# Performance work log

Hardware: AMD Instinct MI355X
Metric: run time of the kernel (lower is better)

Reference implementation:

```python
import jax, jax.numpy as jnp
import numpy as np

N = 100000
E = 1600000
EPS = 1e-16
NEG_SLOPE = 0.2


def setup_inputs() -> dict:
    key = jax.random.key(0)
    ks = jax.random.split(key, 10)
    F_in, C = 512, 40
    H1, D1 = 8, 8
    return {
        "x": jax.random.normal(ks[0], (N, F_in), jnp.float32),
        "edge_index": jax.random.randint(ks[1], (2, E), 0, N, jnp.int64),
        "W1": jax.random.normal(ks[2], (F_in, H1 * D1), jnp.float32) * 0.05,
        "att_src1": jax.random.normal(ks[3], (H1, D1), jnp.float32) * 0.1,
        "att_dst1": jax.random.normal(ks[4], (H1, D1), jnp.float32) * 0.1,
        "b1": jnp.zeros((H1 * D1,), jnp.float32),
        "W2": jax.random.normal(ks[5], (H1 * D1, C), jnp.float32) * 0.05,
        "att_src2": jax.random.normal(ks[6], (1, C), jnp.float32) * 0.1,
        "att_dst2": jax.random.normal(ks[7], (1, C), jnp.float32) * 0.1,
        "b2": jnp.zeros((C,), jnp.float32),
    }


def gat_conv(x, W, att_src, att_dst, bias, src, dst, heads, out_dim, concat):
    # Linear transform per head: [N, H, D]
    h = (x @ W).reshape(N, heads, out_dim)
    # Per-node attention logits: [N, H]
    a_src = jnp.einsum("nhd,hd->nh", h, att_src)
    a_dst = jnp.einsum("nhd,hd->nh", h, att_dst)
    # Per-edge logits (edge j->i: src=j, softmax grouped by dst=i)
    e = a_src[src] + a_dst[dst]                      # [E', H]
    e = jax.nn.leaky_relu(e, NEG_SLOPE)
    # Segment softmax over destination nodes (numerically stable)
    m = jax.ops.segment_max(e, dst, num_segments=N)  # [N, H]
    e = jnp.exp(e - m[dst])
    s = jax.ops.segment_sum(e, dst, num_segments=N)  # [N, H]
    alpha = e / (s[dst] + EPS)                       # [E', H]
    # Weighted message aggregation (scatter-add)
    msg = h[src] * alpha[:, :, None]                 # [E', H, D]
    out = jax.ops.segment_sum(msg, dst, num_segments=N)  # [N, H, D]
    out = out.reshape(N, heads * out_dim) if concat else out.mean(axis=1)
    return out + bias


def reference(x, edge_index, W1, att_src1, att_dst1, b1, W2, att_src2, att_dst2, b2):
    # PyG GATConv default: add self-loops
    loops = jnp.arange(N, dtype=edge_index.dtype)
    src = jnp.concatenate([edge_index[0], loops])
    dst = jnp.concatenate([edge_index[1], loops])
    h = gat_conv(x, W1, att_src1, att_dst1, b1, src, dst, heads=8, out_dim=8, concat=True)
    h = jax.nn.elu(h)
    out = gat_conv(h, W2, att_src2, att_dst2, b2, src, dst, heads=1, out_dim=40, concat=False)
    return jax.nn.log_softmax(out, axis=1)
```

## Files before the change

### kernel.cpp

```cpp
#include <hip/hip_runtime.h>
#include <cstdint>

#define N_NODES 100000
#define N_EDGES 1600000
#define ETOT    1700000
#define FIN     512
#define HD1     64
#define C2      40
#define NEG_SLOPE 0.2f
#define SCAN_NB ((N_NODES + 1023) / 1024)

typedef __attribute__((ext_vector_type(8))) short bf16x8;
typedef __attribute__((ext_vector_type(4))) float f32x4;

__device__ __forceinline__ float lrelu(float v) { return v > 0.f ? v : NEG_SLOPE * v; }

__device__ __forceinline__ unsigned short f2bf(float f) {
    uint32_t u = __float_as_uint(f);
    u += 0x7FFF + ((u >> 16) & 1);
    return (unsigned short)(u >> 16);
}
__device__ __forceinline__ float bf2f(unsigned short u) {
    return __uint_as_float(((uint32_t)u) << 16);
}

__global__ void k_prep(const float* __restrict__ W1, const float* __restrict__ a_s,
                       const float* __restrict__ a_d,
                       const float* __restrict__ W2, const float* __restrict__ att_s2,
                       const float* __restrict__ att_d2,
                       unsigned short* __restrict__ W1t, unsigned short* __restrict__ W2t,
                       int* __restrict__ deg) {
    int i = blockIdx.x * 256 + threadIdx.x;
    if (i < N_NODES) deg[i] = 0;
    if (i < 80 * 512) {
        int n = i >> 9, k = i & 511;
        float v;
        if (n < 64) {
            v = W1[k * HD1 + n];
        } else if (n < 72) {
            int h = n - 64; v = 0.f;
#pragma unroll
            for (int d = 0; d < 8; d++) v += W1[k * HD1 + h * 8 + d] * a_s[h * 8 + d];
        } else {
            int h = n - 72; v = 0.f;
#pragma unroll
            for (int d = 0; d < 8; d++) v += W1[k * HD1 + h * 8 + d] * a_d[h * 8 + d];
        }
        W1t[n * FIN + k] = f2bf(v);
    } else if (i < 80 * 512 + 48 * 64) {
        int j = i - 80 * 512;
        int n = j >> 6, k = j & 63;
        float v = 0.f;
        if (n < C2) {
            v = W2[k * C2 + n];
        } else if (n == C2) {
            for (int c = 0; c < C2; c++) v += W2[k * C2 + c] * att_s2[c];
        } else if (n == C2 + 1) {
            for (int c = 0; c < C2; c++) v += W2[k * C2 + c] * att_d2[c];
        }
        W2t[n * 64 + k] = f2bf(v);
    }
}

__global__ __launch_bounds__(256) void k_gemm1(const float* __restrict__ x,
                                               const unsigned short* __restrict__ W1t,
                                               unsigned short* __restrict__ h1b,
                                               float* __restrict__ as1,
                                               float* __restrict__ ad1) {
    __shared__ unsigned short As[128 * 72];
    const int t    = threadIdx.x;
    const int lane = t & 63, wv = t >> 6;
    const int quad = lane >> 4, l16 = lane & 15;
    const int row0 = blockIdx.x * 128;

    f32x4 acc[2][5];
#pragma unroll
    for (int mi = 0; mi < 2; mi++)
#pragma unroll
        for (int ni = 0; ni < 5; ni++) acc[mi][ni] = (f32x4){0.f, 0.f, 0.f, 0.f};

    float4 rx[8];
#pragma unroll
    for (int i = 0; i < 8; i++) {
        int ff = t + i * 256;
        int r = ff >> 4, c4 = ff & 15;
        int row = row0 + r;
        rx[i] = (row < N_NODES) ? *(const float4*)&x[(size_t)row * FIN + c4 * 4]
                                : make_float4(0.f, 0.f, 0.f, 0.f);
    }

    for (int c = 0; c < 8; c++) {
#pragma unroll
        for (int i = 0; i < 8; i++) {
            int ff = t + i * 256;
            int r = ff >> 4, c4 = ff & 15;
            ushort4 s4;
            s4.x = f2bf(rx[i].x); s4.y = f2bf(rx[i].y);
            s4.z = f2bf(rx[i].z); s4.w = f2bf(rx[i].w);
            *(ushort4*)&As[r * 72 + c4 * 4] = s4;
        }
        __syncthreads();
        if (c < 7) {
            int kb = (c + 1) * 64;
#pragma unroll
            for (int i = 0; i < 8; i++) {
                int ff = t + i * 256;
                int r = ff >> 4, c4 = ff & 15;
                int row = row0 + r;
                rx[i] = (row < N_NODES) ? *(const float4*)&x[(size_t)row * FIN + kb + c4 * 4]
                                        : make_float4(0.f, 0.f, 0.f, 0.f);
            }
        }
        int kb = c * 64;
#pragma unroll
        for (int ks = 0; ks < 2; ks++) {
            bf16x8 af[2], bfv[5];
#pragma unroll
            for (int mi = 0; mi < 2; mi++) {
                int lr = wv * 32 + mi * 16 + l16;
                af[mi] = *(const bf16x8*)&As[lr * 72 + ks * 32 + quad * 8];
            }
#pragma unroll
            for (int ni = 0; ni < 5; ni++) {
                int n = ni * 16 + l16;
                bfv[ni] = *(const bf16x8*)&W1t[n * FIN + kb + ks * 32 + quad * 8];
            }
#pragma unroll
            for (int mi = 0; mi < 2; mi++)
#pragma unroll
                for (int ni = 0; ni < 5; ni++)
                    acc[mi][ni] = __builtin_amdgcn_mfma_f32_16x16x32_bf16(
                        af[mi], bfv[ni], acc[mi][ni], 0, 0, 0);
        }
        __syncthreads();
    }
#pragma unroll
    for (int mi = 0; mi < 2; mi++)
#pragma unroll
        for (int ni = 0; ni < 5; ni++)
#pragma unroll
            for (int r = 0; r < 4; r++) {
                int row = row0 + wv * 32 + mi * 16 + quad * 4 + r;
                if (row >= N_NODES) continue;
                int col = ni * 16 + l16;
                float v = acc[mi][ni][r];
                if (col < 64)       h1b[(size_t)row * 64 + col] = f2bf(v);
                else if (col < 72)  as1[row * 8 + (col - 64)] = v;
                else                ad1[row * 8 + (col - 72)] = v;
            }
}

__global__ void k_degord(const int* __restrict__ ei, int* __restrict__ deg,
                         int* __restrict__ ord) {
    int e = blockIdx.x * 256 + threadIdx.x;
    if (e >= ETOT) return;
    int dst = (e < N_EDGES) ? ei[N_EDGES + e] : e - N_EDGES;
    ord[e] = atomicAdd(&deg[dst], 1);
}

__global__ __launch_bounds__(1024) void k_bsum(const int* __restrict__ deg,
                                               int* __restrict__ bsum) {
    __shared__ int wsm[16];
    int t = threadIdx.x;
    int i = blockIdx.x * 1024 + t;
    int v = (i < N_NODES) ? deg[i] : 0;
#pragma unroll
    for (int o = 32; o >= 1; o >>= 1) v += __shfl_xor(v, o, 64);
    if ((t & 63) == 0) wsm[t >> 6] = v;
    __syncthreads();
    if (t < 16) {
        int s = wsm[t];
#pragma unroll
        for (int o = 8; o >= 1; o >>= 1) s += __shfl_xor(s, o, 16);
        if (t == 0) bsum[blockIdx.x] = s;
    }
}

__global__ __launch_bounds__(128) void k_bscan(const int* __restrict__ bsum,
                                               int* __restrict__ boff) {
    __shared__ int sh[128];
    int t = threadIdx.x;
    int v = (t < SCAN_NB) ? bsum[t] : 0;
    sh[t] = v;
    __syncthreads();
    for (int off = 1; off < 128; off <<= 1) {
        int u = (t >= off) ? sh[t - off] : 0;
        __syncthreads();
        sh[t] += u;
        __syncthreads();
    }
    boff[t] = sh[t] - v;
}

__global__ __launch_bounds__(1024) void k_scan3(const int* __restrict__ deg,
                                                const int* __restrict__ boff,
                                                int* __restrict__ row_ptr) {
    __shared__ int sh[1024];
    int t = threadIdx.x;
    int i = blockIdx.x * 1024 + t;
    int v = (i < N_NODES) ? deg[i] : 0;
    sh[t] = v;
    __syncthreads();
    for (int off = 1; off < 1024; off <<= 1) {
        int u = (t >= off) ? sh[t - off] : 0;
        __syncthreads();
        sh[t] += u;
        __syncthreads();
    }
    int base = boff[blockIdx.x];
    if (i < N_NODES) row_ptr[i] = base + sh[t] - v;
    if (i == N_NODES - 1) row_ptr[N_NODES] = base + sh[t];
}

__global__ void k_scatter(const int* __restrict__ ei, const int* __restrict__ row_ptr,
                          const int* __restrict__ ord, int* __restrict__ csr_src) {
    int e = blockIdx.x * 256 + threadIdx.x;
    if (e >= ETOT) return;
    int src, dst;
    if (e < N_EDGES) { src = ei[e]; dst = ei[N_EDGES + e]; }
    else             { src = dst = e - N_EDGES; }
    csr_src[row_ptr[dst] + ord[e]] = src;
}

__global__ __launch_bounds__(256) void k_agg1(
    const unsigned short* __restrict__ h1b,
    const float* __restrict__ as1, const float* __restrict__ ad1,
    const int* __restrict__ row_ptr, const int* __restrict__ csr_src,
    const float* __restrict__ b1, unsigned short* __restrict__ hb) {
    int t = threadIdx.x, wv = t >> 6, lane = t & 63;
    int dst = blockIdx.x * 4 + wv;
    if (dst >= N_NODES) return;
    int g = lane >> 3, i8 = lane & 7;
    int s0 = row_ptr[dst], s1e = row_ptr[dst + 1];
    float adh = ad1[dst * 8 + i8];
    float den = 0.f;
    float facc[8];
#pragma unroll
    for (int d = 0; d < 8; d++) facc[d] = 0.f;

    for (int base = s0; base < s1e; base += 64) {
        int idx = base + lane;
        int sl = (idx < s1e) ? csr_src[idx] : 0;
        int cnt = min(64, s1e - base);
        for (int j = 0; j < cnt; j += 8) {
            int s = __shfl(sl, j + g);
            bool vld = (j + g) < cnt;
            float w = vld ? __expf(lrelu(as1[s * 8 + i8] + adh)) : 0.f;
            den += w;
            bf16x8 hrow = *(const bf16x8*)&h1b[(size_t)s * 64 + i8 * 8];
#pragma unroll
            for (int d = 0; d < 8; d++)
                facc[d] += w * bf2f((unsigned short)hrow[d]);
        }
    }
#pragma unroll
    for (int o = 8; o <= 32; o <<= 1) {
        den += __shfl_xor(den, o, 64);
#pragma unroll
        for (int d = 0; d < 8; d++) facc[d] += __shfl_xor(facc[d], o, 64);
    }
    float rden = 1.f / (den + 1e-16f);
    float4 b1lo = *(const float4*)&b1[i8 * 8];
    float4 b1hi = *(const float4*)&b1[i8 * 8 + 4];
    float bb[8] = {b1lo.x, b1lo.y, b1lo.z, b1lo.w, b1hi.x, b1hi.y, b1hi.z, b1hi.w};
    bf16x8 pk;
#pragma unroll
    for (int d = 0; d < 8; d++) {
        float hv = facc[d] * rden + bb[d];
        hv = hv > 0.f ? hv : expm1f(hv);
        pk[d] = (short)f2bf(hv);
    }
    if (g == 0) *(bf16x8*)&hb[(size_t)dst * 64 + i8 * 8] = pk;
}

__global__ __launch_bounds__(256) void k_gemm2(const unsigned short* __restrict__ hb,
                                               const unsigned short* __restrict__ W2t,
                                               unsigned short* __restrict__ h2b,
                                               float* __restrict__ as2,
                                               float* __restrict__ ad2) {
    const int t = threadIdx.x;
    const int lane = t & 63, wv = t >> 6;
    const int quad = lane >> 4, l16 = lane & 15;
    const int row0 = blockIdx.x * 128;

    f32x4 acc[2][3];
#pragma unroll
    for (int mi = 0; mi < 2; mi++)
#pragma unroll
        for (int ni = 0; ni < 3; ni++) acc[mi][ni] = (f32x4){0.f, 0.f, 0.f, 0.f};

    bf16x8 bfrag[2][3];
#pragma unroll
    for (int ks = 0; ks < 2; ks++)
#pragma unroll
        for (int ni = 0; ni < 3; ni++)
            bfrag[ks][ni] = *(const bf16x8*)&W2t[(ni * 16 + l16) * 64 + ks * 32 + quad * 8];

#pragma unroll
    for (int mi = 0; mi < 2; mi++) {
        int row = row0 + wv * 32 + mi * 16 + l16;
        int rowc = row < N_NODES ? row : N_NODES - 1;
#pragma unroll
        for (int ks = 0; ks < 2; ks++) {
            bf16x8 af = *(const bf16x8*)&hb[(size_t)rowc * 64 + ks * 32 + quad * 8];
#pragma unroll
            for (int ni = 0; ni < 3; ni++)
                acc[mi][ni] = __builtin_amdgcn_mfma_f32_16x16x32_bf16(
                    af, bfrag[ks][ni], acc[mi][ni], 0, 0, 0);
        }
    }
#pragma unroll
    for (int mi = 0; mi < 2; mi++)
#pragma unroll
        for (int ni = 0; ni < 3; ni++)
#pragma unroll
            for (int r = 0; r < 4; r++) {
                int row = row0 + wv * 32 + mi * 16 + quad * 4 + r;
                if (row >= N_NODES) continue;
                int col = ni * 16 + l16;
                float v = acc[mi][ni][r];
                if (col < C2)            h2b[(size_t)row * C2 + col] = f2bf(v);
                else if (col == C2)      as2[row] = v;
                else if (col == C2 + 1)  ad2[row] = v;
            }
}

__global__ __launch_bounds__(256) void k_agg2(
    const unsigned short* __restrict__ h2b,
    const float* __restrict__ as2, const float* __restrict__ ad2,
    const int* __restrict__ row_ptr, const int* __restrict__ csr_src,
    const float* __restrict__ b2, float* __restrict__ out) {
    int t = threadIdx.x, wv = t >> 6, lane = t & 63;
    int dst = blockIdx.x * 4 + wv;
    if (dst >= N_NODES) return;
    int g = lane >> 3, i8 = lane & 7;
    bool act = i8 < 5;
    int off = act ? i8 * 8 : 0;
    int s0 = row_ptr[dst], s1e = row_ptr[dst + 1];
    float ad = ad2[dst];
    float denp = 0.f;
    float facc[8];
#pragma unroll
    for (int d = 0; d < 8; d++) facc[d] = 0.f;

    for (int base = s0; base < s1e; base += 64) {
        int idx = base + lane;
        int sl = (idx < s1e) ? csr_src[idx] : 0;
        int cnt = min(64, s1e - base);
        for (int j = 0; j < cnt; j += 8) {
            int s = __shfl(sl, j + g);
            bool vld = (j + g) < cnt;
            float wf = vld ? __expf(lrelu(as2[s] + ad)) : 0.f;
            if (i8 == 0) denp += wf;
            float w = act ? wf : 0.f;
            bf16x8 hrow = *(const bf16x8*)&h2b[(size_t)s * C2 + off];
#pragma unroll
            for (int d = 0; d < 8; d++)
                facc[d] += w * bf2f((unsigned short)hrow[d]);
        }
    }
#pragma unroll
    for (int o = 8; o <= 32; o <<= 1)
#pragma unroll
        for (int d = 0; d < 8; d++) facc[d] += __shfl_xor(facc[d], o, 64);
    float den = denp;
#pragma unroll
    for (int o = 32; o >= 1; o >>= 1) den += __shfl_xor(den, o, 64);
    float rden = 1.f / (den + 1e-16f);

    float vch[8];
    float mx = -1e30f;
#pragma unroll
    for (int d = 0; d < 8; d++) {
        vch[d] = act ? facc[d] * rden + b2[off + d] : -1e30f;
        mx = fmaxf(mx, vch[d]);
    }
#pragma unroll
    for (int o = 1; o <= 4; o <<= 1) mx = fmaxf(mx, __shfl_xor(mx, o, 64));
    float es = 0.f;
#pragma unroll
    for (int d = 0; d < 8; d++) es += act ? __expf(vch[d] - mx) : 0.f;
#pragma unroll
    for (int o = 1; o <= 4; o <<= 1) es += __shfl_xor(es, o, 64);
    float lg = logf(es);
    if (g == 0 && act) {
        float4 o0 = {vch[0] - mx - lg, vch[1] - mx - lg, vch[2] - mx - lg, vch[3] - mx - lg};
        float4 o1 = {vch[4] - mx - lg, vch[5] - mx - lg, vch[6] - mx - lg, vch[7] - mx - lg};
        *(float4*)&out[(size_t)dst * C2 + i8 * 8]     = o0;
        *(float4*)&out[(size_t)dst * C2 + i8 * 8 + 4] = o1;
    }
}

extern "C" void kernel_launch(void* const* d_in, const int* in_sizes, int n_in,
                              void* d_out, int out_size, void* d_ws, size_t ws_size,
                              hipStream_t stream) {
    const float* x     = (const float*)d_in[0];
    const int*   ei    = (const int*)d_in[1];
    const float* W1    = (const float*)d_in[2];
    const float* at_s1 = (const float*)d_in[3];
    const float* at_d1 = (const float*)d_in[4];
    const float* b1    = (const float*)d_in[5];
    const float* W2    = (const float*)d_in[6];
    const float* at_s2 = (const float*)d_in[7];
    const float* at_d2 = (const float*)d_in[8];
    const float* b2    = (const float*)d_in[9];
    float* out = (float*)d_out;
    float* ws  = (float*)d_ws;

    unsigned short* h1b = (unsigned short*)ws;
    float* as1 = ws + 3200000;
    float* ad1 = ws + 4000000;
    unsigned short* hb  = (unsigned short*)(ws + 4800000);
    unsigned short* h2b = (unsigned short*)(ws + 8000000);
    float* as2 = ws + 10000000;
    float* ad2 = ws + 10100000;
    unsigned short* W1t = (unsigned short*)(ws + 10200000);
    unsigned short* W2t = (unsigned short*)(ws + 10250000);
    int* row_ptr = (int*)(ws + 10300000);
    int* deg     = (int*)(ws + 10410000);
    int* csr_src = (int*)(ws + 10630000);
    int* bsum    = (int*)(ws + 12340000);
    int* boff    = (int*)(ws + 12350000);
    int* ord     = (int*)(ws + 13000000);

    k_prep<<<391, 256, 0, stream>>>(W1, at_s1, at_d1, W2, at_s2, at_d2, W1t, W2t, deg);
    k_degord<<<(ETOT + 255) / 256, 256, 0, stream>>>(ei, deg, ord);
    k_bsum<<<SCAN_NB, 1024, 0, stream>>>(deg, bsum);
    k_bscan<<<1, 128, 0, stream>>>(bsum, boff);
    k_scan3<<<SCAN_NB, 1024, 0, stream>>>(deg, boff, row_ptr);
    k_scatter<<<(ETOT + 255) / 256, 256, 0, stream>>>(ei, row_ptr, ord, csr_src);
    k_gemm1<<<(N_NODES + 127) / 128, 256, 0, stream>>>(x, W1t, h1b, as1, ad1);
    k_agg1<<<(N_NODES + 3) / 4, 256, 0, stream>>>(h1b, as1, ad1, row_ptr, csr_src, b1, hb);
    k_gemm2<<<(N_NODES + 127) / 128, 256, 0, stream>>>(hb, W2t, h2b, as2, ad2);
    k_agg2<<<(N_NODES + 3) / 4, 256, 0, stream>>>(h2b, as2, ad2, row_ptr, csr_src, b2, out);
}
```

Before: 593.6 us.

## Fuse degree counting into GEMM1 launch, single-pass lookback scan, unroll aggregation

Merges the edge-degree atomic counting into the GEMM1 kernel as extra blocks, so the bandwidth-bound GEMM and the atomic-bound counting run concurrently in one launch. Replaces the three-kernel scan (block sums, block-sum scan, final scan) with a single decoupled-lookback scan that spins on per-block flags. The aggregation loops in both layers now process two neighbours per iteration to expose more memory-level parallelism. The lookback relies on earlier blocks being scheduled first, which holds for 98 blocks on this device. The two-neighbour loop also raises register pressure.

```diff
diff --git a/kernel.cpp b/kernel.cpp
--- a/kernel.cpp
+++ b/kernel.cpp
@@ -8,7 +8,9 @@
 #define HD1     64
 #define C2      40
 #define NEG_SLOPE 0.2f
-#define SCAN_NB ((N_NODES + 1023) / 1024)
+#define GEMM1_NB 782
+#define DEG_NB   832
+#define SCAN_NB2 98
 
 typedef __attribute__((ext_vector_type(8))) short bf16x8;
 typedef __attribute__((ext_vector_type(4))) float f32x4;
@@ -29,9 +31,10 @@
                        const float* __restrict__ W2, const float* __restrict__ att_s2,
                        const float* __restrict__ att_d2,
                        unsigned short* __restrict__ W1t, unsigned short* __restrict__ W2t,
-                       int* __restrict__ deg) {
+                       int* __restrict__ deg, unsigned int* __restrict__ flags) {
     int i = blockIdx.x * 256 + threadIdx.x;
     if (i < N_NODES) deg[i] = 0;
+    if (i < 128) flags[i] = 0u;
     if (i < 80 * 512) {
         int n = i >> 9, k = i & 511;
         float v;
@@ -62,13 +65,23 @@
     }
 }
 
-__global__ __launch_bounds__(256) void k_gemm1(const float* __restrict__ x,
+__global__ __launch_bounds__(256) void k_g1deg(const float* __restrict__ x,
                                                const unsigned short* __restrict__ W1t,
                                                unsigned short* __restrict__ h1b,
                                                float* __restrict__ as1,
-                                               float* __restrict__ ad1) {
+                                               float* __restrict__ ad1,
+                                               const int* __restrict__ ei,
+                                               int* __restrict__ deg,
+                                               int* __restrict__ ord) {
     __shared__ unsigned short As[128 * 72];
-    const int t    = threadIdx.x;
+    const int t = threadIdx.x;
+    if (blockIdx.x >= GEMM1_NB) {
+        for (int e = ((int)blockIdx.x - GEMM1_NB) * 256 + t; e < ETOT; e += DEG_NB * 256) {
+            int dst = (e < N_EDGES) ? ei[N_EDGES + e] : e - N_EDGES;
+            ord[e] = atomicAdd(&deg[dst], 1);
+        }
+        return;
+    }
     const int lane = t & 63, wv = t >> 6;
     const int quad = lane >> 4, l16 = lane & 15;
     const int row0 = blockIdx.x * 128;
@@ -150,54 +163,15 @@
             }
 }
 
-__global__ void k_degord(const int* __restrict__ ei, int* __restrict__ deg,
-                         int* __restrict__ ord) {
-    int e = blockIdx.x * 256 + threadIdx.x;
-    if (e >= ETOT) return;
-    int dst = (e < N_EDGES) ? ei[N_EDGES + e] : e - N_EDGES;
-    ord[e] = atomicAdd(&deg[dst], 1);
-}
-
-__global__ __launch_bounds__(1024) void k_bsum(const int* __restrict__ deg,
-                                               int* __restrict__ bsum) {
-    __shared__ int wsm[16];
-    int t = threadIdx.x;
-    int i = blockIdx.x * 1024 + t;
-    int v = (i < N_NODES) ? deg[i] : 0;
-#pragma unroll
-    for (int o = 32; o >= 1; o >>= 1) v += __shfl_xor(v, o, 64);
-    if ((t & 63) == 0) wsm[t >> 6] = v;
-    __syncthreads();
-    if (t < 16) {
-        int s = wsm[t];
-#pragma unroll
-        for (int o = 8; o >= 1; o >>= 1) s += __shfl_xor(s, o, 16);
-        if (t == 0) bsum[blockIdx.x] = s;
-    }
-}
-
-__global__ __launch_bounds__(128) void k_bscan(const int* __restrict__ bsum,
-                                               int* __restrict__ boff) {
-    __shared__ int sh[128];
-    int t = threadIdx.x;
-    int v = (t < SCAN_NB) ? bsum[t] : 0;
-    sh[t] = v;
-    __syncthreads();
-    for (int off = 1; off < 128; off <<= 1) {
-        int u = (t >= off) ? sh[t - off] : 0;
-        __syncthreads();
-        sh[t] += u;
-        __syncthreads();
-    }
-    boff[t] = sh[t] - v;
-}
-
-__global__ __launch_bounds__(1024) void k_scan3(const int* __restrict__ deg,
-                                                const int* __restrict__ boff,
-                                                int* __restrict__ row_ptr) {
+__global__ __launch_bounds__(1024) void k_scan_lb(const int* __restrict__ deg,
+                                                  int* __restrict__ row_ptr,
+                                                  int* __restrict__ aggr,
+                                                  int* __restrict__ incl,
+                                                  unsigned int* __restrict__ flags) {
     __shared__ int sh[1024];
-    int t = threadIdx.x;
-    int i = blockIdx.x * 1024 + t;
+    __shared__ int shbase;
+    const int t = threadIdx.x, b = blockIdx.x;
+    const int i = b * 1024 + t;
     int v = (i < N_NODES) ? deg[i] : 0;
     sh[t] = v;
     __syncthreads();
@@ -207,9 +181,39 @@
         sh[t] += u;
         __syncthreads();
     }
-    int base = boff[blockIdx.x];
+    if (t == 0) {
+        int total = sh[1023];
+        int run = 0;
+        if (b == 0) {
+            __hip_atomic_store(&incl[0], total, __ATOMIC_RELEASE, __HIP_MEMORY_SCOPE_AGENT);
+            __hip_atomic_store(&flags[0], 2u, __ATOMIC_RELEASE, __HIP_MEMORY_SCOPE_AGENT);
+        } else {
+            __hip_atomic_store(&aggr[b], total, __ATOMIC_RELEASE, __HIP_MEMORY_SCOPE_AGENT);
+            __hip_atomic_store(&flags[b], 1u, __ATOMIC_RELEASE, __HIP_MEMORY_SCOPE_AGENT);
+            int p = b - 1;
+            while (true) {
+                unsigned int f = __hip_atomic_load(&flags[p], __ATOMIC_ACQUIRE,
+                                                   __HIP_MEMORY_SCOPE_AGENT);
+                if (f == 2u) {
+                    run += __hip_atomic_load(&incl[p], __ATOMIC_ACQUIRE,
+                                             __HIP_MEMORY_SCOPE_AGENT);
+                    break;
+                } else if (f == 1u) {
+                    run += __hip_atomic_load(&aggr[p], __ATOMIC_ACQUIRE,
+                                             __HIP_MEMORY_SCOPE_AGENT);
+                    --p;
+                }
+            }
+            __hip_atomic_store(&incl[b], run + total, __ATOMIC_RELEASE,
+                               __HIP_MEMORY_SCOPE_AGENT);
+            __hip_atomic_store(&flags[b], 2u, __ATOMIC_RELEASE, __HIP_MEMORY_SCOPE_AGENT);
+        }
+        shbase = run;
+        if (b == 0) row_ptr[N_NODES] = ETOT;
+    }
+    __syncthreads();
+    int base = shbase;
     if (i < N_NODES) row_ptr[i] = base + sh[t] - v;
-    if (i == N_NODES - 1) row_ptr[N_NODES] = base + sh[t];
 }
 
 __global__ void k_scatter(const int* __restrict__ ei, const int* __restrict__ row_ptr,
@@ -242,15 +246,21 @@
         int idx = base + lane;
         int sl = (idx < s1e) ? csr_src[idx] : 0;
         int cnt = min(64, s1e - base);
-        for (int j = 0; j < cnt; j += 8) {
-            int s = __shfl(sl, j + g);
-            bool vld = (j + g) < cnt;
-            float w = vld ? __expf(lrelu(as1[s * 8 + i8] + adh)) : 0.f;
-            den += w;
-            bf16x8 hrow = *(const bf16x8*)&h1b[(size_t)s * 64 + i8 * 8];
+        for (int j = 0; j < cnt; j += 16) {
+            int sA = __shfl(sl, j + g);
+            int sB = __shfl(sl, j + 8 + g);
+            bool vA = (j + g) < cnt, vB = (j + 8 + g) < cnt;
+            bf16x8 rA = *(const bf16x8*)&h1b[(size_t)sA * 64 + i8 * 8];
+            bf16x8 rB = *(const bf16x8*)&h1b[(size_t)sB * 64 + i8 * 8];
+            float aA = as1[sA * 8 + i8];
+            float aB = as1[sB * 8 + i8];
+            float wA = vA ? __expf(lrelu(aA + adh)) : 0.f;
+            float wB = vB ? __expf(lrelu(aB + adh)) : 0.f;
+            den += wA + wB;
 #pragma unroll
             for (int d = 0; d < 8; d++)
-                facc[d] += w * bf2f((unsigned short)hrow[d]);
+                facc[d] += wA * bf2f((unsigned short)rA[d]) +
+                           wB * bf2f((unsigned short)rB[d]);
         }
     }
 #pragma unroll
@@ -347,16 +357,23 @@
         int idx = base + lane;
         int sl = (idx < s1e) ? csr_src[idx] : 0;
         int cnt = min(64, s1e - base);
-        for (int j = 0; j < cnt; j += 8) {
-            int s = __shfl(sl, j + g);
-            bool vld = (j + g) < cnt;
-            float wf = vld ? __expf(lrelu(as2[s] + ad)) : 0.f;
-            if (i8 == 0) denp += wf;
-            float w = act ? wf : 0.f;
-            bf16x8 hrow = *(const bf16x8*)&h2b[(size_t)s * C2 + off];
+        for (int j = 0; j < cnt; j += 16) {
+            int sA = __shfl(sl, j + g);
+            int sB = __shfl(sl, j + 8 + g);
+            bool vA = (j + g) < cnt, vB = (j + 8 + g) < cnt;
+            bf16x8 rA = *(const bf16x8*)&h2b[(size_t)sA * C2 + off];
+            bf16x8 rB = *(const bf16x8*)&h2b[(size_t)sB * C2 + off];
+            float aA = as2[sA];
+            float aB = as2[sB];
+            float wfA = vA ? __expf(lrelu(aA + ad)) : 0.f;
+            float wfB = vB ? __expf(lrelu(aB + ad)) : 0.f;
+            if (i8 == 0) denp += wfA + wfB;
+            float wA = act ? wfA : 0.f;
+            float wB = act ? wfB : 0.f;
 #pragma unroll
             for (int d = 0; d < 8; d++)
-                facc[d] += w * bf2f((unsigned short)hrow[d]);
+                facc[d] += wA * bf2f((unsigned short)rA[d]) +
+                           wB * bf2f((unsigned short)rB[d]);
         }
     }
 #pragma unroll
@@ -419,17 +436,15 @@
     int* row_ptr = (int*)(ws + 10300000);
     int* deg     = (int*)(ws + 10410000);
     int* csr_src = (int*)(ws + 10630000);
-    int* bsum    = (int*)(ws + 12340000);
-    int* boff    = (int*)(ws + 12350000);
+    int* aggrA   = (int*)(ws + 12340000);
+    int* inclA   = (int*)(ws + 12350000);
+    unsigned int* flags = (unsigned int*)(ws + 12360000);
     int* ord     = (int*)(ws + 13000000);
 
-    k_prep<<<391, 256, 0, stream>>>(W1, at_s1, at_d1, W2, at_s2, at_d2, W1t, W2t, deg);
-    k_degord<<<(ETOT + 255) / 256, 256, 0, stream>>>(ei, deg, ord);
-    k_bsum<<<SCAN_NB, 1024, 0, stream>>>(deg, bsum);
-    k_bscan<<<1, 128, 0, stream>>>(bsum, boff);
-    k_scan3<<<SCAN_NB, 1024, 0, stream>>>(deg, boff, row_ptr);
+    k_prep<<<391, 256, 0, stream>>>(W1, at_s1, at_d1, W2, at_s2, at_d2, W1t, W2t, deg, flags);
+    k_g1deg<<<GEMM1_NB + DEG_NB, 256, 0, stream>>>(x, W1t, h1b, as1, ad1, ei, deg, ord);
+    k_scan_lb<<<SCAN_NB2, 1024, 0, stream>>>(deg, row_ptr, aggrA, inclA, flags);
     k_scatter<<<(ETOT + 255) / 256, 256, 0, stream>>>(ei, row_ptr, ord, csr_src);
-    k_gemm1<<<(N_NODES + 127) / 128, 256, 0, stream>>>(x, W1t, h1b, as1, ad1);
     k_agg1<<<(N_NODES + 3) / 4, 256, 0, stream>>>(h1b, as1, ad1, row_ptr, csr_src, b1, hb);
     k_gemm2<<<(N_NODES + 127) / 128, 256, 0, stream>>>(hb, W2t, h2b, as2, ad2);
     k_agg2<<<(N_NODES + 3) / 4, 256, 0, stream>>>(h2b, as2, ad2, row_ptr, csr_src, b2, out);
```

Result: faster. 565.7 us (-4.7%).
